# Performance work log

Measured on AMD Instinct MI355X. Metric: run time of the kernel, lower is better.

## Reference

```python
import jax, jax.numpy as jnp
import numpy as np

N, CX, CS, H = 2048, 768, 384, 16
D = CX // H  # 48


def _ln(t, eps=1e-5):
    mu = jnp.mean(t, axis=-1, keepdims=True)
    var = jnp.mean(jnp.square(t - mu), axis=-1, keepdims=True)
    return (t - mu) * jax.lax.rsqrt(var + eps)


def setup_inputs() -> dict:
    key = jax.random.key(0)
    ks = jax.random.split(key, 16)
    s = 0.02
    return {
        "x": jax.random.normal(ks[0], (N, CX), jnp.float32),
        "mask": jax.random.randint(ks[1], (N,), 0, 2, jnp.int32),
        "pair_logits": jax.random.normal(ks[2], (H, N, N), jnp.float32),
        "single_cond": jax.random.normal(ks[3], (N, CS), jnp.float32),
        # AdaptiveLayerNorm params (single_cond LN has weight, no bias)
        "ln_sc_w": jnp.ones((CS,), jnp.float32),
        "sc_scale_w": s * jax.random.normal(ks[4], (CS, CX), jnp.float32),
        "sc_scale_b": jnp.zeros((CX,), jnp.float32),
        "sc_bias_w": s * jax.random.normal(ks[5], (CS, CX), jnp.float32),
        # q/k/v/gating projections (stored as (in, out); y = x @ W)
        "q_w": s * jax.random.normal(ks[6], (CX, CX), jnp.float32),
        "q_b": jnp.zeros((CX,), jnp.float32),
        "k_w": s * jax.random.normal(ks[7], (CX, CX), jnp.float32),
        "v_w": s * jax.random.normal(ks[8], (CX, CX), jnp.float32),
        "gate_w": s * jax.random.normal(ks[9], (CX, CX), jnp.float32),
        # AdaLNZero params
        "out_w": s * jax.random.normal(ks[10], (CX, CX), jnp.float32),
        "azc_w": s * jax.random.normal(ks[11], (CS, CX), jnp.float32),
        "azc_b": jnp.zeros((CX,), jnp.float32),
    }


def reference(x, mask, pair_logits, single_cond, ln_sc_w, sc_scale_w, sc_scale_b,
              sc_bias_w, q_w, q_b, k_w, v_w, gate_w, out_w, azc_w, azc_b):
    # AdaptiveLayerNorm (use_single_cond=True)
    xn = _ln(x)                              # (N, CX), no affine
    sc = _ln(single_cond) * ln_sc_w          # (N, CS), weight only
    xa = jax.nn.sigmoid(sc @ sc_scale_w + sc_scale_b) * xn + sc @ sc_bias_w

    # QKV projections, split into heads: (N, H, D)
    q = (xa @ q_w + q_b).reshape(N, H, D)
    k = (xa @ k_w).reshape(N, H, D)
    v = (xa @ v_w).reshape(N, H, D)

    # Attention with per-head additive pair bias and key mask
    logits = jnp.einsum("qhd,khd->hqk", q * (D ** -0.5), k) + pair_logits
    logits = jnp.where(mask.astype(bool)[None, None, :], logits, -1e9)
    w = jax.nn.softmax(logits, axis=-1)      # (H, N, N)
    wa = jnp.einsum("hqk,khd->qhd", w, v).reshape(N, CX)

    # Gating, then AdaLNZero output
    wa = wa * jax.nn.sigmoid(xa @ gate_w)
    out = (wa @ out_w) * jax.nn.sigmoid(sc @ azc_w + azc_b)
    return out
```

## Files before the change

### kernel.cpp

```cpp
#include <hip/hip_runtime.h>
#include <math.h>

#define NN 2048
#define CXX 768
#define CSS 384
#define HH 16
#define DHH 48
#define KSPLIT 4

typedef short bf16x8 __attribute__((ext_vector_type(8)));
typedef float f32x4 __attribute__((ext_vector_type(4)));

#define MFMA16(a,b,c) __builtin_amdgcn_mfma_f32_16x16x32_bf16(a,b,c,0,0,0)

__device__ __forceinline__ unsigned short f2bf(float f){
  unsigned u = __float_as_uint(f);
  u += 0x7FFFu + ((u >> 16) & 1u);
  return (unsigned short)(u >> 16);
}
__device__ __forceinline__ float bf2f(unsigned short u){
  return __uint_as_float(((unsigned)u) << 16);
}
__device__ __forceinline__ void async_copy16(const void* g, void* l){
  __builtin_amdgcn_global_load_lds((const __attribute__((address_space(1))) void*)g,
                                   (__attribute__((address_space(3))) void*)l, 16, 0, 0);
}

__device__ inline float waveReduceSum(float v){
  #pragma unroll
  for(int o=32;o>0;o>>=1) v += __shfl_xor(v,o);
  return v;
}

__global__ __launch_bounds__(256) void transpose_all(
    const float* __restrict__ s0, const float* __restrict__ s1, const float* __restrict__ s2,
    const float* __restrict__ s3, const float* __restrict__ s4, const float* __restrict__ s5,
    const float* __restrict__ s6, const float* __restrict__ s7,
    unsigned short* __restrict__ d_scale, unsigned short* __restrict__ d_bias,
    unsigned short* __restrict__ d_azc, unsigned short* __restrict__ d_qkvg,
    unsigned short* __restrict__ d_out){
  int z = blockIdx.z;
  const float* W; unsigned short* Wt; int K;
  switch(z){
    case 0: W=s0; Wt=d_scale; K=384; break;
    case 1: W=s1; Wt=d_bias;  K=384; break;
    case 2: W=s2; Wt=d_azc;   K=384; break;
    case 3: W=s3; Wt=d_qkvg + 0*589824; K=768; break;
    case 4: W=s4; Wt=d_qkvg + 1*589824; K=768; break;
    case 5: W=s5; Wt=d_qkvg + 2*589824; K=768; break;
    case 6: W=s6; Wt=d_qkvg + 3*589824; K=768; break;
    default: W=s7; Wt=d_out; K=768; break;
  }
  int n0 = blockIdx.x*32, k0 = blockIdx.y*32;
  if(k0 >= K) return;
  __shared__ unsigned short t[32][33];
  int c = threadIdx.x & 31, r = threadIdx.x >> 5;
  #pragma unroll
  for(int i=0;i<32;i+=8){
    float v = W[(size_t)(k0 + r + i)*CXX + n0 + c];
    t[c][r+i] = f2bf(v);
  }
  __syncthreads();
  #pragma unroll
  for(int i=0;i<32;i+=8){
    Wt[(size_t)(n0 + r + i)*K + k0 + c] = t[r+i][c];
  }
}

__global__ __launch_bounds__(384) void ln_fused(const float* __restrict__ x,
    const float* __restrict__ scin, const float* __restrict__ w,
    float* __restrict__ xn, unsigned short* __restrict__ scb){
  int row = blockIdx.x;
  int t = threadIdx.x;
  int wid = t>>6, lane = t&63;
  __shared__ float red[6];
  float a0 = x[(size_t)row*CXX + t];
  float a1 = x[(size_t)row*CXX + 384 + t];
  float s = waveReduceSum(a0+a1);
  if(lane==0) red[wid]=s;
  __syncthreads();
  float mu = (red[0]+red[1]+red[2]+red[3]+red[4]+red[5]) * (1.0f/CXX);
  float d0=a0-mu, d1=a1-mu;
  float q = waveReduceSum(d0*d0+d1*d1);
  __syncthreads();
  if(lane==0) red[wid]=q;
  __syncthreads();
  float var = (red[0]+red[1]+red[2]+red[3]+red[4]+red[5]) * (1.0f/CXX);
  float r = rsqrtf(var + 1e-5f);
  xn[(size_t)row*CXX + t] = d0*r;
  xn[(size_t)row*CXX + 384 + t] = d1*r;
  float b = scin[(size_t)row*CSS + t];
  float s2 = waveReduceSum(b);
  __syncthreads();
  if(lane==0) red[wid]=s2;
  __syncthreads();
  float mu2 = (red[0]+red[1]+red[2]+red[3]+red[4]+red[5]) * (1.0f/CSS);
  float d2 = b - mu2;
  float q2 = waveReduceSum(d2*d2);
  __syncthreads();
  if(lane==0) red[wid]=q2;
  __syncthreads();
  float var2 = (red[0]+red[1]+red[2]+red[3]+red[4]+red[5]) * (1.0f/CSS);
  float r2 = rsqrtf(var2 + 1e-5f);
  scb[(size_t)row*CSS + t] = f2bf(d2*r2*w[t]);
}

__global__ __launch_bounds__(256) void gemm_qkvg(const unsigned short* __restrict__ A,
    const unsigned short* __restrict__ Bt, const float* __restrict__ bias,
    unsigned short* __restrict__ C, unsigned short* __restrict__ vt){
  __shared__ unsigned short As[128*32];
  __shared__ unsigned short Bs[128*32];
  const int tid = threadIdx.x;
  const int w = tid>>6, lane = tid&63;
  const int ln15 = lane&15, hi = lane>>4;
  const int wm = w&1, wn = w>>1;
  const int m0 = blockIdx.y*128, n0 = blockIdx.x*128;
  const int lrow = lane>>2, lk = (lane&3)*8;
  const int K = 768, NC = 3072;

  f32x4 z = {0.f,0.f,0.f,0.f};
  f32x4 acc[4][4];
  #pragma unroll
  for(int i=0;i<4;i++)
    #pragma unroll
    for(int j=0;j<4;j++) acc[i][j] = z;

  for(int k0=0;k0<K;k0+=32){
    const unsigned short* ga = A + (size_t)(m0 + w*32 + lrow)*K + k0 + lk;
    const unsigned short* gb = Bt + (size_t)(n0 + w*32 + lrow)*K + k0 + lk;
    async_copy16(ga,          &As[w*1024]);
    async_copy16(ga + 16*K,   &As[w*1024 + 512]);
    async_copy16(gb,          &Bs[w*1024]);
    async_copy16(gb + 16*K,   &Bs[w*1024 + 512]);
    __syncthreads();
    bf16x8 af[4], bfr[4];
    #pragma unroll
    for(int i=0;i<4;i++) af[i]  = *(const bf16x8*)&As[(wm*64 + i*16 + ln15)*32 + hi*8];
    #pragma unroll
    for(int j=0;j<4;j++) bfr[j] = *(const bf16x8*)&Bs[(wn*64 + j*16 + ln15)*32 + hi*8];
    #pragma unroll
    for(int i=0;i<4;i++)
      #pragma unroll
      for(int j=0;j<4;j++)
        acc[i][j] = MFMA16(af[i], bfr[j], acc[i][j]);
    __syncthreads();
  }

  #pragma unroll
  for(int i=0;i<4;i++)
    #pragma unroll
    for(int j=0;j<4;j++){
      int gm0 = m0 + wm*64 + i*16 + hi*4;
      int gn  = n0 + wn*64 + j*16 + ln15;
      if(gn >= 1536 && gn < 2304){
        ushort4 v4;
        v4.x = f2bf(acc[i][j][0]);
        v4.y = f2bf(acc[i][j][1]);
        v4.z = f2bf(acc[i][j][2]);
        v4.w = f2bf(acc[i][j][3]);
        *(ushort4*)&vt[(size_t)(gn - 1536)*NN + gm0] = v4;
      } else {
        #pragma unroll
        for(int r=0;r<4;r++){
          float v = acc[i][j][r];
          if(gn < 768) v += bias[gn];
          if(gn >= 2304) v = 1.0f/(1.0f + __expf(-v));
          C[(size_t)(gm0+r)*NC + gn] = f2bf(v);
        }
      }
    }
}

__global__ __launch_bounds__(256) void adaln3(const unsigned short* __restrict__ A,
    const unsigned short* __restrict__ B1, const unsigned short* __restrict__ B2,
    const unsigned short* __restrict__ B3, const float* __restrict__ bs,
    const float* __restrict__ zb, const float* __restrict__ xn,
    unsigned short* __restrict__ xa, float* __restrict__ azc){
  __shared__ unsigned short As[64*32];
  __shared__ unsigned short Bs1[64*32];
  __shared__ unsigned short Bs2[64*32];
  __shared__ unsigned short Bs3[64*32];
  const int tid = threadIdx.x;
  const int w = tid>>6, lane = tid&63;
  const int ln15 = lane&15, hi = lane>>4;
  const int wm = w&1, wn = w>>1;
  const int m0 = blockIdx.y*64, n0 = blockIdx.x*64;
  const int lrow = tid>>2, lk = (tid&3)*8;
  const int K = CSS;

  f32x4 z = {0.f,0.f,0.f,0.f};
  f32x4 acc1[2][2], acc2[2][2], acc3[2][2];
  #pragma unroll
  for(int i=0;i<2;i++)
    #pragma unroll
    for(int j=0;j<2;j++){ acc1[i][j]=z; acc2[i][j]=z; acc3[i][j]=z; }

  for(int k0=0;k0<K;k0+=32){
    async_copy16(A  + (size_t)(m0+lrow)*K + k0 + lk, &As [w*512]);
    async_copy16(B1 + (size_t)(n0+lrow)*K + k0 + lk, &Bs1[w*512]);
    async_copy16(B2 + (size_t)(n0+lrow)*K + k0 + lk, &Bs2[w*512]);
    async_copy16(B3 + (size_t)(n0+lrow)*K + k0 + lk, &Bs3[w*512]);
    __syncthreads();
    bf16x8 af[2], b1f[2], b2f[2], b3f[2];
    #pragma unroll
    for(int i=0;i<2;i++) af[i]  = *(const bf16x8*)&As[(wm*32 + i*16 + ln15)*32 + hi*8];
    #pragma unroll
    for(int j=0;j<2;j++){
      b1f[j] = *(const bf16x8*)&Bs1[(wn*32 + j*16 + ln15)*32 + hi*8];
      b2f[j] = *(const bf16x8*)&Bs2[(wn*32 + j*16 + ln15)*32 + hi*8];
      b3f[j] = *(const bf16x8*)&Bs3[(wn*32 + j*16 + ln15)*32 + hi*8];
    }
    #pragma unroll
    for(int i=0;i<2;i++)
      #pragma unroll
      for(int j=0;j<2;j++){
        acc1[i][j] = MFMA16(af[i], b1f[j], acc1[i][j]);
        acc2[i][j] = MFMA16(af[i], b2f[j], acc2[i][j]);
        acc3[i][j] = MFMA16(af[i], b3f[j], acc3[i][j]);
      }
    __syncthreads();
  }

  #pragma unroll
  for(int i=0;i<2;i++)
    #pragma unroll
    for(int j=0;j<2;j++)
      #pragma unroll
      for(int r=0;r<4;r++){
        int gm = m0 + wm*32 + i*16 + hi*4 + r;
        int gn = n0 + wn*32 + j*16 + ln15;
        float g = 1.0f/(1.0f + __expf(-(acc1[i][j][r] + bs[gn])));
        float v = g * xn[(size_t)gm*CXX + gn] + acc2[i][j][r];
        xa[(size_t)gm*CXX + gn] = f2bf(v);
        azc[(size_t)gm*CXX + gn] = 1.0f/(1.0f + __expf(-(acc3[i][j][r] + zb[gn])));
      }
}

__global__ __launch_bounds__(256) void gemm_out(const unsigned short* __restrict__ A,
    const unsigned short* __restrict__ Bt, const float* __restrict__ mul,
    float* __restrict__ C){
  __shared__ unsigned short As[64*32];
  __shared__ unsigned short Bs[64*32];
  const int tid = threadIdx.x;
  const int w = tid>>6, lane = tid&63;
  const int ln15 = lane&15, hi = lane>>4;
  const int wm = w&1, wn = w>>1;
  const int m0 = blockIdx.y*64, n0 = blockIdx.x*64;
  const int lrow = tid>>2, lk = (tid&3)*8;
  const int K = 768;

  f32x4 z = {0.f,0.f,0.f,0.f};
  f32x4 acc[2][2];
  #pragma unroll
  for(int i=0;i<2;i++)
    #pragma unroll
    for(int j=0;j<2;j++) acc[i][j]=z;

  for(int k0=0;k0<K;k0+=32){
    async_copy16(A  + (size_t)(m0+lrow)*K + k0 + lk, &As[w*512]);
    async_copy16(Bt + (size_t)(n0+lrow)*K + k0 + lk, &Bs[w*512]);
    __syncthreads();
    bf16x8 af[2], bfr[2];
    #pragma unroll
    for(int i=0;i<2;i++) af[i]  = *(const bf16x8*)&As[(wm*32 + i*16 + ln15)*32 + hi*8];
    #pragma unroll
    for(int j=0;j<2;j++) bfr[j] = *(const bf16x8*)&Bs[(wn*32 + j*16 + ln15)*32 + hi*8];
    #pragma unroll
    for(int i=0;i<2;i++)
      #pragma unroll
      for(int j=0;j<2;j++)
        acc[i][j] = MFMA16(af[i], bfr[j], acc[i][j]);
    __syncthreads();
  }

  #pragma unroll
  for(int i=0;i<2;i++)
    #pragma unroll
    for(int j=0;j<2;j++)
      #pragma unroll
      for(int r=0;r<4;r++){
        int gm = m0 + wm*32 + i*16 + hi*4 + r;
        int gn = n0 + wn*32 + j*16 + ln15;
        C[(size_t)gm*CXX + gn] = acc[i][j][r] * mul[(size_t)gm*CXX + gn];
      }
}


#define ATTN_STEP(KF0C, KF1C, PFC, KF0N, KF1N, KK, KNXT, KP2) do{                  \
    int4 mk[4];                                                                    \
    _Pragma("unroll")                                                              \
    for(int jt=0;jt<4;jt++) mk[jt] = *(const int4*)&mask[(KK) + jt*16 + hi*4];     \
    bf16x8 vf0[3], vf1[3];                                                         \
    _Pragma("unroll")                                                              \
    for(int dt=0;dt<3;dt++){                                                       \
      const unsigned short* vp_ = vt + (size_t)(h*DHH + dt*16 + ln15)*NN + (KK) + hi*8; \
      vf0[dt] = *(const bf16x8*)vp_;                                               \
      vf1[dt] = *(const bf16x8*)(vp_ + 32);                                        \
    }                                                                              \
    f32x4 sreg[4];                                                                 \
    __builtin_amdgcn_s_setprio(1);                                                 \
    _Pragma("unroll")                                                              \
    for(int jt=0;jt<4;jt++){                                                       \
      f32x4 s_ = z;                                                                \
      s_ = MFMA16(KF0C[jt], bq0, s_);                                              \
      s_ = MFMA16(KF1C[jt], bq1, s_);                                              \
      sreg[jt] = s_;                                                               \
    }                                                                              \
    __builtin_amdgcn_s_setprio(0);                                                 \
    _Pragma("unroll")                                                              \
    for(int jt=0;jt<4;jt++){                                                       \
      const unsigned short* kp_ = qkvg + (size_t)((KNXT) + jt*16 + ln15)*3072 + 768 + h*DHH + hi*8; \
      KF0N[jt] = *(const bf16x8*)kp_;                                              \
      KF1N[jt] = *(const bf16x8*)(kp_ + 32);                                       \
    }                                                                              \
    float sv[4][4];                                                                \
    _Pragma("unroll")                                                              \
    for(int jt=0;jt<4;jt++){                                                       \
      sv[jt][0] = mk[jt].x ? sreg[jt][0]*scale + PFC[jt].x : -1e9f;                \
      sv[jt][1] = mk[jt].y ? sreg[jt][1]*scale + PFC[jt].y : -1e9f;                \
      sv[jt][2] = mk[jt].z ? sreg[jt][2]*scale + PFC[jt].z : -1e9f;                \
      sv[jt][3] = mk[jt].w ? sreg[jt][3]*scale + PFC[jt].w : -1e9f;                \
    }                                                                              \
    _Pragma("unroll")                                                              \
    for(int jt=0;jt<4;jt++)                                                        \
      PFC[jt] = *(const float4*)&pbase[(KP2) + jt*16 + hi*4];                      \
    float vmax = sv[0][0];                                                         \
    _Pragma("unroll")                                                              \
    for(int jt=0;jt<4;jt++)                                                        \
      _Pragma("unroll")                                                            \
      for(int r=0;r<4;r++) vmax = fmaxf(vmax, sv[jt][r]);                          \
    vmax = fmaxf(vmax, __shfl_xor(vmax,16));                                       \
    vmax = fmaxf(vmax, __shfl_xor(vmax,32));                                       \
    float mn = fmaxf(m_run, vmax);                                                 \
    float al = __expf(m_run - mn);                                                 \
    m_run = mn;                                                                    \
    float pv[4][4];                                                                \
    float rs = 0.f;                                                                \
    _Pragma("unroll")                                                              \
    for(int jt=0;jt<4;jt++)                                                        \
      _Pragma("unroll")                                                            \
      for(int r=0;r<4;r++){                                                        \
        pv[jt][r] = __expf(sv[jt][r] - mn);                                        \
        rs += pv[jt][r];                                                           \
      }                                                                            \
    rs += __shfl_xor(rs,16);                                                       \
    rs += __shfl_xor(rs,32);                                                       \
    l_run = l_run*al + rs;                                                         \
    _Pragma("unroll")                                                              \
    for(int jt=0;jt<4;jt++){                                                       \
      unsigned int w0_ = (unsigned)f2bf(pv[jt][0]) | ((unsigned)f2bf(pv[jt][1])<<16); \
      unsigned int w1_ = (unsigned)f2bf(pv[jt][2]) | ((unsigned)f2bf(pv[jt][3])<<16); \
      *(uint2*)&Pme[ln15*36 + jt*8 + hi*2] = make_uint2(w0_,w1_);                  \
    }                                                                              \
    __asm__ volatile("s_waitcnt lgkmcnt(0)" ::: "memory");                         \
    __builtin_amdgcn_sched_barrier(0);                                             \
    _Pragma("unroll")                                                              \
    for(int dt=0;dt<3;dt++)                                                        \
      _Pragma("unroll")                                                            \
      for(int r=0;r<4;r++) oacc[dt][r] *= al;                                      \
    bf16x8 bp0 = *(const bf16x8*)&Pme[ln15*36 + hi*4];                             \
    bf16x8 bp1 = *(const bf16x8*)&Pme[ln15*36 + 16 + hi*4];                        \
    __builtin_amdgcn_s_setprio(1);                                                 \
    _Pragma("unroll")                                                              \
    for(int dt=0;dt<3;dt++){                                                       \
      oacc[dt] = MFMA16(vf0[dt], bp0, oacc[dt]);                                   \
      oacc[dt] = MFMA16(vf1[dt], bp1, oacc[dt]);                                   \
    }                                                                              \
    __builtin_amdgcn_s_setprio(0);                                                 \
  }while(0)

__global__ __launch_bounds__(64) void attn_mfma(const unsigned short* __restrict__ qkvg,
    const unsigned short* __restrict__ vt, const float* __restrict__ pair,
    const int* __restrict__ mask, float* __restrict__ po, float* __restrict__ pm,
    float* __restrict__ pl){
  const int h = blockIdx.y;
  const int q0 = blockIdx.x*16;
  const int kz = blockIdx.z;
  const int kbase = kz*(NN/KSPLIT);
  const int NT = (NN/KSPLIT)/64;
  const int lane = threadIdx.x & 63;
  const int ln15 = lane&15, hi = lane>>4;
  const int q = q0 + ln15;

  __shared__ unsigned int Pme[16*36];

  const float scale = 0.14433756729740643f;
  f32x4 z = {0.f,0.f,0.f,0.f};

  const unsigned short* qp = qkvg + (size_t)q*3072 + h*DHH + hi*8;
  bf16x8 bq0 = *(const bf16x8*)qp;
  bf16x8 bq1 = *(const bf16x8*)(qp + 32);
  if(hi >= 2){ bf16x8 z8 = {0,0,0,0,0,0,0,0}; bq1 = z8; }

  f32x4 oacc[3] = {z,z,z};
  float m_run = -1e30f, l_run = 0.f;

  bf16x8 kf0a[4], kf1a[4], kf0b[4], kf1b[4];
  float4 pfa[4], pfb[4];

  const float* pbase = pair + ((size_t)h*NN + q)*NN;

  #pragma unroll
  for(int jt=0;jt<4;jt++){
    const unsigned short* kp = qkvg + (size_t)(kbase + jt*16 + ln15)*3072 + 768 + h*DHH + hi*8;
    kf0a[jt] = *(const bf16x8*)kp;
    kf1a[jt] = *(const bf16x8*)(kp+32);
    pfa[jt] = *(const float4*)&pbase[kbase + jt*16 + hi*4];
    pfb[jt] = *(const float4*)&pbase[kbase + 64 + jt*16 + hi*4];
  }

  for(int t=0; t<NT; t+=2){
    const int kk = kbase + t*64;
    const int kp2a = (t+2 < NT) ? kk + 128 : kbase;
    const int kp2b = (t+3 < NT) ? kk + 192 : kbase;
    const int knb  = (t+2 < NT) ? kk + 128 : kbase;
    ATTN_STEP(kf0a, kf1a, pfa, kf0b, kf1b, kk,      kk+64, kp2a);
    ATTN_STEP(kf0b, kf1b, pfb, kf0a, kf1a, kk+64,   knb,   kp2b);
  }

  size_t rowi = ((size_t)(kz*HH + h))*NN + q;
  #pragma unroll
  for(int dt=0;dt<3;dt++){
    float4 o4;
    o4.x = oacc[dt][0]; o4.y = oacc[dt][1]; o4.z = oacc[dt][2]; o4.w = oacc[dt][3];
    *(float4*)&po[rowi*DHH + dt*16 + hi*4] = o4;
  }
  if(hi==0){ pm[rowi] = m_run; pl[rowi] = l_run; }
}

__global__ __launch_bounds__(256) void attn_combine(const float* __restrict__ po,
    const float* __restrict__ pm, const float* __restrict__ pl,
    const unsigned short* __restrict__ qkvg, unsigned short* __restrict__ wag){
  const int row = blockIdx.x*4 + (threadIdx.x>>6);
  const int lane = threadIdx.x & 63;
  #pragma unroll
  for(int i=0;i<12;i++){
    int c = lane + i*64;
    int hh = c / DHH, d = c - hh*DHH;
    float mv[KSPLIT];
    float M = -1e30f;
    #pragma unroll
    for(int s=0;s<KSPLIT;s++){
      mv[s] = pm[((size_t)(s*HH + hh))*NN + row];
      M = fmaxf(M, mv[s]);
    }
    float L = 0.f, V = 0.f;
    #pragma unroll
    for(int s=0;s<KSPLIT;s++){
      size_t rr = ((size_t)(s*HH + hh))*NN + row;
      float e = __expf(mv[s] - M);
      L += pl[rr]*e;
      V += po[rr*DHH + d]*e;
    }
    float g = bf2f(qkvg[(size_t)row*3072 + 2304 + c]);
    wag[(size_t)row*CXX + c] = f2bf((V/L) * g);
  }
}

extern "C" void kernel_launch(void* const* d_in, const int* in_sizes, int n_in,
                              void* d_out, int out_size, void* d_ws, size_t ws_size,
                              hipStream_t stream) {
  const float* x           = (const float*)d_in[0];
  const int*   mask        = (const int*)  d_in[1];
  const float* pair        = (const float*)d_in[2];
  const float* single_cond = (const float*)d_in[3];
  const float* ln_sc_w     = (const float*)d_in[4];
  const float* sc_scale_w  = (const float*)d_in[5];
  const float* sc_scale_b  = (const float*)d_in[6];
  const float* sc_bias_w   = (const float*)d_in[7];
  const float* q_w         = (const float*)d_in[8];
  const float* q_b         = (const float*)d_in[9];
  const float* k_w         = (const float*)d_in[10];
  const float* v_w         = (const float*)d_in[11];
  const float* gate_w      = (const float*)d_in[12];
  const float* out_w       = (const float*)d_in[13];
  const float* azc_w       = (const float*)d_in[14];
  const float* azc_b       = (const float*)d_in[15];
  float* out = (float*)d_out;

  unsigned short* p = (unsigned short*)d_ws;
  unsigned short* Wt_scale = p;  p += 768*384;
  unsigned short* Wt_bias  = p;  p += 768*384;
  unsigned short* Wt_azc   = p;  p += 768*384;
  unsigned short* Wt_out   = p;  p += 768*768;
  unsigned short* Wt_qkvg  = p;  p += (size_t)3072*768;
  unsigned short* scb      = p;  p += 2048*384;
  unsigned short* xa       = p;  p += 2048*768;
  unsigned short* qkvg     = p;  p += (size_t)2048*3072;
  unsigned short* wag      = p;  p += 2048*768;
  unsigned short* vt       = p;  p += (size_t)768*2048;
  float* fp = (float*)p;
  float* xn  = fp; fp += (size_t)2048*768;
  float* azc = fp; fp += (size_t)2048*768;
  float* po  = fp; fp += (size_t)KSPLIT*HH*NN*DHH;
  float* pm  = fp; fp += (size_t)KSPLIT*HH*NN;
  float* pl  = fp;

  transpose_all<<<dim3(24,24,8), 256, 0, stream>>>(
      sc_scale_w, sc_bias_w, azc_w, q_w, k_w, v_w, gate_w, out_w,
      Wt_scale, Wt_bias, Wt_azc, Wt_qkvg, Wt_out);

  ln_fused<<<NN, 384, 0, stream>>>(x, single_cond, ln_sc_w, xn, scb);

  adaln3<<<dim3(12,32), 256, 0, stream>>>(scb, Wt_scale, Wt_bias, Wt_azc,
                                          sc_scale_b, azc_b, xn, xa, azc);

  gemm_qkvg<<<dim3(24,16), 256, 0, stream>>>(xa, Wt_qkvg, q_b, qkvg, vt);

  attn_mfma<<<dim3(128,16,KSPLIT), 64, 0, stream>>>(qkvg, vt, pair, mask, po, pm, pl);

  attn_combine<<<512, 256, 0, stream>>>(po, pm, pl, qkvg, wag);

  gemm_out<<<dim3(12,32), 256, 0, stream>>>(wag, Wt_out, azc, out);
}
```

Measured before the change: 568.6 us.

## Stage K and pair-bias tiles into LDS via async global_load_lds double buffering

```diff
diff --git a/kernel.cpp b/kernel.cpp
--- a/kernel.cpp
+++ b/kernel.cpp
@@ -286,7 +286,22 @@
 }
 
 
-#define ATTN_STEP(KF0C, KF1C, PFC, KF0N, KF1N, KK, KNXT, KP2) do{                  \
+#define STAGE(BUF, KK) do{                                                         \
+    _Pragma("unroll")                                                              \
+    for(int j=0;j<6;j++)                                                           \
+      async_copy16(qkvg + (size_t)((KK)+lane)*3072 + 768 + h*DHH + j*8,            \
+                   &Kbuf[BUF][j*512 + lane*8]);                                    \
+    _Pragma("unroll")                                                              \
+    for(int j=0;j<4;j++)                                                           \
+      async_copy16(pair + ((size_t)h*NN + q0 + (lane>>2))*NN + (KK) + (j*4+(lane&3))*4, \
+                   &Pairbuf[BUF][j*256 + lane*4]);                                 \
+  }while(0)
+
+#define ATTN_TILE(CUR, NXT, KK, KNXT, DOSTAGE) do{                                 \
+    __asm__ volatile("s_waitcnt vmcnt(0)" ::: "memory");                           \
+    __builtin_amdgcn_sched_barrier(0);                                             \
+    if(DOSTAGE){ STAGE(NXT, KNXT); }                                               \
+    __builtin_amdgcn_sched_barrier(0);                                             \
     int4 mk[4];                                                                    \
     _Pragma("unroll")                                                              \
     for(int jt=0;jt<4;jt++) mk[jt] = *(const int4*)&mask[(KK) + jt*16 + hi*4];     \
@@ -297,33 +312,31 @@
       vf0[dt] = *(const bf16x8*)vp_;                                               \
       vf1[dt] = *(const bf16x8*)(vp_ + 32);                                        \
     }                                                                              \
+    bf16x8 kf0[4], kf1[4];                                                         \
+    _Pragma("unroll")                                                              \
+    for(int jt=0;jt<4;jt++){                                                       \
+      kf0[jt] = *(const bf16x8*)&Kbuf[CUR][hi*512 + (jt*16+ln15)*8];               \
+      kf1[jt] = *(const bf16x8*)&Kbuf[CUR][(4+(hi&1))*512 + (jt*16+ln15)*8];       \
+    }                                                                              \
     f32x4 sreg[4];                                                                 \
     __builtin_amdgcn_s_setprio(1);                                                 \
     _Pragma("unroll")                                                              \
     for(int jt=0;jt<4;jt++){                                                       \
       f32x4 s_ = z;                                                                \
-      s_ = MFMA16(KF0C[jt], bq0, s_);                                              \
-      s_ = MFMA16(KF1C[jt], bq1, s_);                                              \
+      s_ = MFMA16(kf0[jt], bq0, s_);                                               \
+      s_ = MFMA16(kf1[jt], bq1, s_);                                               \
       sreg[jt] = s_;                                                               \
     }                                                                              \
     __builtin_amdgcn_s_setprio(0);                                                 \
+    float sv[4][4];                                                                \
     _Pragma("unroll")                                                              \
     for(int jt=0;jt<4;jt++){                                                       \
-      const unsigned short* kp_ = qkvg + (size_t)((KNXT) + jt*16 + ln15)*3072 + 768 + h*DHH + hi*8; \
-      KF0N[jt] = *(const bf16x8*)kp_;                                              \
-      KF1N[jt] = *(const bf16x8*)(kp_ + 32);                                       \
+      float4 pq = *(const float4*)&Pairbuf[CUR][jt*256 + (ln15*4+hi)*4];           \
+      sv[jt][0] = mk[jt].x ? sreg[jt][0]*scale + pq.x : -1e9f;                     \
+      sv[jt][1] = mk[jt].y ? sreg[jt][1]*scale + pq.y : -1e9f;                     \
+      sv[jt][2] = mk[jt].z ? sreg[jt][2]*scale + pq.z : -1e9f;                     \
+      sv[jt][3] = mk[jt].w ? sreg[jt][3]*scale + pq.w : -1e9f;                     \
     }                                                                              \
-    float sv[4][4];                                                                \
-    _Pragma("unroll")                                                              \
-    for(int jt=0;jt<4;jt++){                                                       \
-      sv[jt][0] = mk[jt].x ? sreg[jt][0]*scale + PFC[jt].x : -1e9f;                \
-      sv[jt][1] = mk[jt].y ? sreg[jt][1]*scale + PFC[jt].y : -1e9f;                \
-      sv[jt][2] = mk[jt].z ? sreg[jt][2]*scale + PFC[jt].z : -1e9f;                \
-      sv[jt][3] = mk[jt].w ? sreg[jt][3]*scale + PFC[jt].w : -1e9f;                \
-    }                                                                              \
-    _Pragma("unroll")                                                              \
-    for(int jt=0;jt<4;jt++)                                                        \
-      PFC[jt] = *(const float4*)&pbase[(KP2) + jt*16 + hi*4];                      \
     float vmax = sv[0][0];                                                         \
     _Pragma("unroll")                                                              \
     for(int jt=0;jt<4;jt++)                                                        \
@@ -382,6 +395,8 @@
   const int ln15 = lane&15, hi = lane>>4;
   const int q = q0 + ln15;
 
+  __shared__ unsigned short Kbuf[2][3072];
+  __shared__ float Pairbuf[2][1024];
   __shared__ unsigned int Pme[16*36];
 
   const float scale = 0.14433756729740643f;
@@ -395,27 +410,12 @@
   f32x4 oacc[3] = {z,z,z};
   float m_run = -1e30f, l_run = 0.f;
 
-  bf16x8 kf0a[4], kf1a[4], kf0b[4], kf1b[4];
-  float4 pfa[4], pfb[4];
-
-  const float* pbase = pair + ((size_t)h*NN + q)*NN;
-
-  #pragma unroll
-  for(int jt=0;jt<4;jt++){
-    const unsigned short* kp = qkvg + (size_t)(kbase + jt*16 + ln15)*3072 + 768 + h*DHH + hi*8;
-    kf0a[jt] = *(const bf16x8*)kp;
-    kf1a[jt] = *(const bf16x8*)(kp+32);
-    pfa[jt] = *(const float4*)&pbase[kbase + jt*16 + hi*4];
-    pfb[jt] = *(const float4*)&pbase[kbase + 64 + jt*16 + hi*4];
-  }
+  STAGE(0, kbase);
 
   for(int t=0; t<NT; t+=2){
     const int kk = kbase + t*64;
-    const int kp2a = (t+2 < NT) ? kk + 128 : kbase;
-    const int kp2b = (t+3 < NT) ? kk + 192 : kbase;
-    const int knb  = (t+2 < NT) ? kk + 128 : kbase;
-    ATTN_STEP(kf0a, kf1a, pfa, kf0b, kf1b, kk,      kk+64, kp2a);
-    ATTN_STEP(kf0b, kf1b, pfb, kf0a, kf1a, kk+64,   knb,   kp2b);
+    ATTN_TILE(0, 1, kk,      kk+64,  1);
+    ATTN_TILE(1, 0, kk+64,   kk+128, (t+2 < NT));
   }
 
   size_t rowi = ((size_t)(kz*HH + h))*NN + q;
```

New measurement: 575.6 us. Within noise of the previous version (+1.2%).
